# Kernel tuning notes

Measured on AMD Instinct MI355X. Metric: run time of the kernel, lower is better.

Reference implementation:

```python
import jax, jax.numpy as jnp
import numpy as np

B, F, O = 32, 26, 20
IN, G = 2048, 512
REL = 53
EPS = 1e-5  # BatchNorm1d default eps


def setup_inputs() -> dict:
    key = jax.random.key(0)
    ks = jax.random.split(key, 10)
    inp = {
        "region_feats": jax.random.normal(ks[0], (B, F, O, IN), jnp.float32),
        "region_masks": jnp.ones((B, F, O), jnp.float32),
        "rel_feats": jax.random.randint(ks[1], (B, F, O, O), 0, REL, jnp.int64),
        "tem_feats": jax.random.uniform(ks[2], (B, F * O, F * O), jnp.float32),
        # learned params (eval mode: dropout off, BN uses running stats)
        "rel_W": jax.random.normal(ks[3], (G, IN), jnp.float32) * (1.0 / np.sqrt(IN)),
        "rel_b": jnp.zeros((G,), jnp.float32),
        "rel_emb": jax.random.normal(ks[4], (REL, G), jnp.float32) * 0.02,
        "tem_W": jax.random.normal(ks[5], (G, IN), jnp.float32) * (1.0 / np.sqrt(IN)),
        "tem_b": jnp.zeros((G,), jnp.float32),
        "bn_w": jnp.ones((F * O,), jnp.float32),
        "bn_b": jnp.zeros((F * O,), jnp.float32),
        "bn_rm": jnp.zeros((F * O,), jnp.float32),
        "bn_rv": jnp.ones((F * O,), jnp.float32),
    }
    return inp


def reference(region_feats, region_masks, rel_feats, tem_feats,
              rel_W, rel_b, rel_emb, tem_W, tem_b,
              bn_w, bn_b, bn_rm, bn_rv):
    b, f, o, _ = region_feats.shape
    # ---- RELATIONAL FEATURE GRAPH ----
    # [B,F,O,G]
    rel_region = jnp.einsum("bfoi,gi->bfog", region_feats, rel_W) + rel_b
    # embedding lookup: [B,F,O,O,G]
    emb = rel_emb[rel_feats]
    mask = (rel_feats > 0).astype(region_feats.dtype)  # [B,F,O,O]
    msum = jnp.sum(mask, axis=3)                        # [B,F,O]
    # sum_j mask_ij * emb_ij  (masked reduction over neighbor dim)
    emb_sum = jnp.einsum("bfijg,bfij->bfig", emb, mask)
    # sum_j mask_ij * r_i == r_i * msum_i, so (emb_sum + r*msum)/msum
    rel_out = (emb_sum + rel_region * msum[..., None]) / msum[..., None]
    rel_out = rel_out.reshape(b, f * o, -1)
    # ---- TEMPORAL FEATURE GRAPH ----
    tem_region = jnp.einsum("bfoi,gi->bfog", region_feats, tem_W) + tem_b
    tem_region = tem_region.reshape(b, f * o, -1)
    tem_sum = jnp.sum(tem_feats, axis=2)                # [B, F*O]
    tem_out = jnp.matmul(tem_feats, tem_region) / tem_sum[..., None]
    # ---- OUTPUT ----
    out = jnp.concatenate([rel_out, tem_out], axis=-1)  # [B, F*O, 2G]
    out = jnp.tanh(out)
    # BatchNorm1d over channel dim 1 (eval mode, running stats)
    inv = bn_w / jnp.sqrt(bn_rv + EPS)                  # [F*O]
    out = (out - bn_rm[None, :, None]) * inv[None, :, None] + bn_b[None, :, None]
    return out
```

## Files before the change

### kernel.cpp

```cpp
#include <hip/hip_runtime.h>
#include <stdint.h>

#define BB 32
#define FO 520
#define M1 16640
#define KIN 2048
#define KA 2112
#define N1 1024
#define GG 512
#define K2P 576
#define M2 640

typedef unsigned short u16;
typedef short v8s __attribute__((ext_vector_type(8)));
typedef float v4f __attribute__((ext_vector_type(4)));

__device__ __forceinline__ u16 f2bf(float f) {
  union { float f; unsigned u; } v; v.f = f;
  unsigned r = v.u + 0x7fffu + ((v.u >> 16) & 1u);
  return (u16)(r >> 16);
}

__device__ __forceinline__ float fast_tanh(float x) {
  float cx = fminf(fmaxf(x, -15.f), 15.f);
  float e = __expf(2.f * cx);
  return (e - 1.f) / (e + 1.f);
}

__device__ __forceinline__ void glds(const u16* g, u16* l) {
  __builtin_amdgcn_global_load_lds((const __attribute__((address_space(1))) void*)g,
                                   (__attribute__((address_space(3))) void*)l, 16, 0, 0);
}

#define PREP_ROWS 8832
__global__ __launch_bounds__(512) void prep_all_kernel(
    const float* __restrict__ rf, const int* __restrict__ rel,
    const float* __restrict__ relW, const float* __restrict__ temW,
    const float* __restrict__ emb, const float* __restrict__ tem,
    u16* __restrict__ A1, u16* __restrict__ Wc,
    u16* __restrict__ A2, float* __restrict__ tsum) {
  const int blk = blockIdx.x;
  const int t = threadIdx.x;
  if (blk < PREP_ROWS) {
    const int row = blk * 2 + (t >> 8);
    const int tt = t & 255;
    const float* src;
    u16* orow;
    if (row < M1) { src = rf + (size_t)row * KIN; orow = A1 + (size_t)row * KA; }
    else {
      const int n = row - M1;
      src = (n < GG) ? (relW + (size_t)n * KIN) : (temW + (size_t)(n - GG) * KIN);
      orow = Wc + (size_t)n * KA;
    }
    const v4f* p = (const v4f*)src;
    v4f a = __builtin_nontemporal_load(p + 2 * tt);
    v4f b = __builtin_nontemporal_load(p + 2 * tt + 1);
    v8s v;
    v[0] = (short)f2bf(a[0]); v[1] = (short)f2bf(a[1]);
    v[2] = (short)f2bf(a[2]); v[3] = (short)f2bf(a[3]);
    v[4] = (short)f2bf(b[0]); v[5] = (short)f2bf(b[1]);
    v[6] = (short)f2bf(b[2]); v[7] = (short)f2bf(b[3]);
    *(v8s*)(orow + tt * 8) = v;
    if (tt < 64) {
      float sval = 0.f;
      if (row < M1) {
        const int* rp = rel + (size_t)row * 20;
        int cnt = 0, ms = 0;
#pragma unroll
        for (int j = 0; j < 20; ++j) { int ix = rp[j]; cnt += (ix == tt + 1); ms += (ix > 0); }
        if (tt < 52 && ms > 0) sval = (float)cnt / (float)ms;
      } else {
        const int n = row - M1;
        if (n < GG && tt < 52) sval = emb[(size_t)(tt + 1) * GG + n];
      }
      orow[KIN + tt] = f2bf(sval);
    }
    return;
  }
  const int w = t >> 6, l = t & 63;
  const int row = (blk - PREP_ROWS) * 8 + w;
  const int b = row / M2, i = row % M2;
  u16* orow = A2 + (size_t)row * K2P;
  v8s z = {0, 0, 0, 0, 0, 0, 0, 0};
  if (i >= FO) {
    *(v8s*)(orow + l * 8) = z;
    if (l < 8) *(v8s*)(orow + (64 + l) * 8) = z;
    return;
  }
  const float* srow = tem + ((size_t)b * FO + i) * FO;
  float s = 0.f;
  {
    v4f a = __builtin_nontemporal_load((const v4f*)(srow + 8 * l));
    v4f bb = __builtin_nontemporal_load((const v4f*)(srow + 8 * l + 4));
    s += a[0] + a[1] + a[2] + a[3] + bb[0] + bb[1] + bb[2] + bb[3];
    v8s v;
    v[0] = (short)f2bf(a[0]); v[1] = (short)f2bf(a[1]);
    v[2] = (short)f2bf(a[2]); v[3] = (short)f2bf(a[3]);
    v[4] = (short)f2bf(bb[0]); v[5] = (short)f2bf(bb[1]);
    v[6] = (short)f2bf(bb[2]); v[7] = (short)f2bf(bb[3]);
    *(v8s*)(orow + l * 8) = v;
  }
  if (l < 8) {
    if (l == 0) {
      v4f a = __builtin_nontemporal_load((const v4f*)(srow + 512));
      v4f bb = __builtin_nontemporal_load((const v4f*)(srow + 516));
      s += a[0] + a[1] + a[2] + a[3] + bb[0] + bb[1] + bb[2] + bb[3];
      v8s v;
      v[0] = (short)f2bf(a[0]); v[1] = (short)f2bf(a[1]);
      v[2] = (short)f2bf(a[2]); v[3] = (short)f2bf(a[3]);
      v[4] = (short)f2bf(bb[0]); v[5] = (short)f2bf(bb[1]);
      v[6] = (short)f2bf(bb[2]); v[7] = (short)f2bf(bb[3]);
      *(v8s*)(orow + 512) = v;
    } else {
      *(v8s*)(orow + (64 + l) * 8) = z;
    }
  }
#pragma unroll
  for (int off = 32; off > 0; off >>= 1) s += __shfl_down(s, off);
  if (l == 0) tsum[(size_t)b * FO + i] = s;
}

#define G1_STAGE(DST)                                                                            \
  do {                                                                                           \
    u16* dst_ = smem + (DST) + tid * 8;                                                          \
    glds(ga0, dst_);         glds(ga1, dst_ + 2048);                                             \
    glds(ga2, dst_ + 4096);  glds(ga3, dst_ + 6144);                                             \
    glds(gb0, dst_ + 8192);  glds(gb1, dst_ + 10240);                                            \
    ga0 += 32; ga1 += 32; ga2 += 32; ga3 += 32; gb0 += 32; gb1 += 32;                            \
  } while (0)

#define G1_COMPUTE(CB)                                                                           \
  do {                                                                                           \
    const u16* As_ = smem + (CB) * 12288;                                                        \
    const u16* Bs_ = As_ + 8192;                                                                 \
    v8s af[8], bf[4];                                                                            \
    _Pragma("unroll") for (int i = 0; i < 8; ++i) {                                              \
      const int ra = wm * 128 + i * 16 + r16;                                                    \
      af[i] = *(const v8s*)&As_[ra * 32 + ((quad ^ ((ra >> 1) & 3)) * 8)];                       \
    }                                                                                            \
    _Pragma("unroll") for (int j = 0; j < 4; ++j) {                                              \
      const int rb = wn * 64 + j * 16 + r16;                                                     \
      bf[j] = *(const v8s*)&Bs_[rb * 32 + ((quad ^ ((rb >> 1) & 3)) * 8)];                       \
    }                                                                                            \
    _Pragma("unroll") for (int i = 0; i < 8; ++i)                                                \
      _Pragma("unroll") for (int j = 0; j < 4; ++j)                                              \
        acc[i][j] =                                                                              \
            __builtin_amdgcn_mfma_f32_16x16x32_bf16(af[i], bf[j], acc[i][j], 0, 0, 0);           \
  } while (0)

__global__ __launch_bounds__(256, 2) void gemm1_kernel(
    const u16* __restrict__ A, const u16* __restrict__ Wc,
    const float* __restrict__ rel_b, const float* __restrict__ tem_b,
    const float* __restrict__ bn_w, const float* __restrict__ bn_b,
    const float* __restrict__ bn_rm, const float* __restrict__ bn_rv,
    float* __restrict__ out, u16* __restrict__ BT) {
  __shared__ u16 smem[36864];
  const int tid = threadIdx.x;
  const int lane = tid & 63;
  const int wv = tid >> 6, wm = wv >> 1, wn = wv & 1;
  const int id = blockIdx.x;
  const int wgid = (id & 7) * 65 + (id >> 3);
  const int mt = wgid >> 3, nt = wgid & 7;
  const int m0 = mt * 256, n0 = nt * 128;
  const int quad = lane >> 4, r16 = lane & 15;

  const u16 *ga0, *ga1, *ga2, *ga3, *gb0, *gb1;
  {
    const int r0 = tid >> 2, sl0 = tid & 3;
    const int c0 = (sl0 ^ ((r0 >> 1) & 3)) * 8;
    ga0 = A + (size_t)(m0 + r0) * KA + c0;
    ga1 = A + (size_t)(m0 + 64 + r0) * KA + c0;
    ga2 = A + (size_t)(m0 + 128 + r0) * KA + c0;
    ga3 = A + (size_t)(m0 + 192 + r0) * KA + c0;
    gb0 = Wc + (size_t)(n0 + r0) * KA + c0;
    gb1 = Wc + (size_t)(n0 + 64 + r0) * KA + c0;
  }

  v4f acc[8][4];
#pragma unroll
  for (int i = 0; i < 8; ++i)
#pragma unroll
    for (int j = 0; j < 4; ++j) { v4f z = {0.f, 0.f, 0.f, 0.f}; acc[i][j] = z; }

  G1_STAGE(0);
  G1_STAGE(12288);

  int cb = 0, nb = 2;
  for (int t = 0; t < 64; ++t) {
    G1_STAGE(nb * 12288);
    asm volatile("s_waitcnt vmcnt(12)" ::: "memory");
    __builtin_amdgcn_s_barrier();
    G1_COMPUTE(cb);
    asm volatile("s_waitcnt lgkmcnt(0)" ::: "memory");
    __builtin_amdgcn_s_barrier();
    cb = (cb == 2) ? 0 : cb + 1;
    nb = (nb == 2) ? 0 : nb + 1;
  }
  {
    const int cb1 = (cb == 2) ? 0 : cb + 1;
    asm volatile("s_waitcnt vmcnt(6)" ::: "memory");
    __builtin_amdgcn_s_barrier();
    G1_COMPUTE(cb);
    asm volatile("s_waitcnt vmcnt(0) lgkmcnt(0)" ::: "memory");
    __builtin_amdgcn_s_barrier();
    G1_COMPUTE(cb1);
  }

  if (n0 < GG) {
#pragma unroll
    for (int mtt = 0; mtt < 8; ++mtt) {
      const int mb = m0 + wm * 128 + mtt * 16 + quad * 4;
      const int bb = mb / FO;
      const int fo0 = mb - bb * FO;
      float inv[4], rm[4], bofs[4];
#pragma unroll
      for (int r = 0; r < 4; ++r) {
        const int fo = fo0 + r;
        inv[r] = bn_w[fo] * rsqrtf(bn_rv[fo] + 1e-5f);
        rm[r] = bn_rm[fo]; bofs[r] = bn_b[fo];
      }
#pragma unroll
      for (int ntt = 0; ntt < 4; ++ntt) {
        const int n = n0 + wn * 64 + ntt * 16 + r16;
        const float rbn = rel_b[n];
#pragma unroll
        for (int r = 0; r < 4; ++r) {
          float val = (fast_tanh(acc[mtt][ntt][r] + rbn) - rm[r]) * inv[r] + bofs[r];
          __builtin_nontemporal_store(val, out + (size_t)(mb + r) * N1 + n);
        }
      }
    }
  } else {
    __syncthreads();
#pragma unroll
    for (int p = 0; p < 2; ++p) {
      if (p) __syncthreads();
      if (wn == p) {
#pragma unroll
        for (int mtt = 0; mtt < 8; ++mtt) {
          const int il = wm * 128 + mtt * 16 + quad * 4;
#pragma unroll
          for (int ntt = 0; ntt < 4; ++ntt) {
            const int gl = ntt * 16 + r16;
            const float tb = tem_b[(n0 - GG) + p * 64 + gl];
            ushort4 w;
            w.x = f2bf(acc[mtt][ntt][0] + tb);
            w.y = f2bf(acc[mtt][ntt][1] + tb);
            w.z = f2bf(acc[mtt][ntt][2] + tb);
            w.w = f2bf(acc[mtt][ntt][3] + tb);
            *(ushort4*)&smem[gl * 264 + il] = w;
          }
        }
      }
      __syncthreads();
#pragma unroll
      for (int pass = 0; pass < 8; ++pass) {
        const int gl = pass * 8 + (tid >> 5);
        const int ch = tid & 31;
        const int m = m0 + ch * 8;
        const int b1 = m / FO;
        const int i1 = m - b1 * FO;
        v8s val = *(const v8s*)&smem[gl * 264 + ch * 8];
        const int g = (n0 - GG) + p * 64 + gl;
        *(v8s*)(BT + ((size_t)(b1 * GG + g)) * K2P + i1) = val;
      }
    }
  }
}

#define G2_STAGE(DST)                                                                            \
  do {                                                                                           \
    u16* dst_ = smem + (DST);                                                                    \
    glds(ga0, dst_ + lofA0); glds(gb0, dst_ + lofB0); glds(gb1, dst_ + lofB1);                   \
    ga0 += 32; gb0 += 32; gb1 += 32;                                                             \
  } while (0)

#define G2_COMPUTE(CB)                                                                           \
  do {                                                                                           \
    const u16* As_ = smem + (CB) * 12288;                                                        \
    const u16* Bs_ = As_ + 4096;                                                                 \
    v8s af[4], bf[4];                                                                            \
    _Pragma("unroll") for (int t4 = 0; t4 < 4; ++t4) {                                           \
      const int ra = wm * 64 + t4 * 16 + r16;                                                    \
      const int rb = wn * 64 + t4 * 16 + r16;                                                    \
      af[t4] = *(const v8s*)&As_[ra * 32 + ((quad ^ ((ra >> 1) & 3)) * 8)];                      \
      bf[t4] = *(const v8s*)&Bs_[rb * 32 + ((quad ^ ((rb >> 1) & 3)) * 8)];                      \
    }                                                                                            \
    _Pragma("unroll") for (int mtt = 0; mtt < 4; ++mtt)                                          \
      _Pragma("unroll") for (int ntt = 0; ntt < 4; ++ntt)                                        \
        acc[mtt][ntt] =                                                                          \
            __builtin_amdgcn_mfma_f32_16x16x32_bf16(af[mtt], bf[ntt], acc[mtt][ntt], 0, 0, 0);   \
  } while (0)

__global__ __launch_bounds__(512, 4) void gemm2_kernel(
    const u16* __restrict__ A2, const u16* __restrict__ BT,
    const float* __restrict__ tsum,
    const float* __restrict__ bn_w, const float* __restrict__ bn_b,
    const float* __restrict__ bn_rm, const float* __restrict__ bn_rv,
    float* __restrict__ out) {
  __shared__ u16 smem[36864];
  const int tid = threadIdx.x;
  const int lane = tid & 63;
  const int wv = tid >> 6, wm = wv >> 2, wn = wv & 3;
  const int m0 = blockIdx.x * 128;
  const int n0 = blockIdx.y * 256;
  const int b = blockIdx.z;
  const u16* Ab = A2 + (size_t)b * M2 * K2P;
  const u16* Bb = BT + (size_t)b * GG * K2P;
  const int quad = lane >> 4, r16 = lane & 15;

  const u16 *ga0, *gb0, *gb1;
  {
    const int r0 = tid >> 2, sl0 = tid & 3;
    const int c0 = (sl0 ^ ((r0 >> 1) & 3)) * 8;
    ga0 = Ab + (size_t)(m0 + r0) * K2P + c0;
    gb0 = Bb + (size_t)(n0 + r0) * K2P + c0;
    gb1 = Bb + (size_t)(n0 + 128 + r0) * K2P + c0;
  }
  const int lofA0 = wv * 512;
  const int lofB0 = 4096 + wv * 512;
  const int lofB1 = 8192 + wv * 512;

  v4f acc[4][4];
#pragma unroll
  for (int i = 0; i < 4; ++i)
#pragma unroll
    for (int j = 0; j < 4; ++j) { v4f z = {0.f, 0.f, 0.f, 0.f}; acc[i][j] = z; }

  G2_STAGE(0);
  G2_STAGE(12288);

  int cb = 0, nb = 2;
  for (int t = 0; t < 16; ++t) {
    G2_STAGE(nb * 12288);
    asm volatile("s_waitcnt vmcnt(6)" ::: "memory");
    __builtin_amdgcn_s_barrier();
    G2_COMPUTE(cb);
    asm volatile("s_waitcnt lgkmcnt(0)" ::: "memory");
    __builtin_amdgcn_s_barrier();
    cb = (cb == 2) ? 0 : cb + 1;
    nb = (nb == 2) ? 0 : nb + 1;
  }
  {
    const int cb1 = (cb == 2) ? 0 : cb + 1;
    asm volatile("s_waitcnt vmcnt(3)" ::: "memory");
    __builtin_amdgcn_s_barrier();
    G2_COMPUTE(cb);
    asm volatile("s_waitcnt vmcnt(0) lgkmcnt(0)" ::: "memory");
    __builtin_amdgcn_s_barrier();
    G2_COMPUTE(cb1);
  }

#pragma unroll
  for (int mtt = 0; mtt < 4; ++mtt) {
    const int ibase = m0 + wm * 64 + mtt * 16 + quad * 4;
    if (ibase >= FO) continue;
    float ts[4], inv[4], rm[4], bofs[4];
#pragma unroll
    for (int r = 0; r < 4; ++r) {
      const int i = ibase + r;
      ts[r] = 1.f / tsum[(size_t)b * FO + i];
      inv[r] = bn_w[i] * rsqrtf(bn_rv[i] + 1e-5f);
      rm[r] = bn_rm[i]; bofs[r] = bn_b[i];
    }
#pragma unroll
    for (int ntt = 0; ntt < 4; ++ntt) {
      const int g = n0 + wn * 64 + ntt * 16 + r16;
#pragma unroll
      for (int r = 0; r < 4; ++r) {
        float val = (fast_tanh(acc[mtt][ntt][r] * ts[r]) - rm[r]) * inv[r] + bofs[r];
        __builtin_nontemporal_store(val, out + ((size_t)(b * FO + (ibase + r))) * N1 + GG + g);
      }
    }
  }
}

extern "C" void kernel_launch(void* const* d_in, const int* in_sizes, int n_in,
                              void* d_out, int out_size, void* d_ws, size_t ws_size,
                              hipStream_t stream) {
  const float* region_feats = (const float*)d_in[0];
  const int* rel_feats = (const int*)d_in[2];
  const float* tem_feats = (const float*)d_in[3];
  const float* rel_W = (const float*)d_in[4];
  const float* rel_b = (const float*)d_in[5];
  const float* rel_emb = (const float*)d_in[6];
  const float* tem_W = (const float*)d_in[7];
  const float* tem_b = (const float*)d_in[8];
  const float* bn_w = (const float*)d_in[9];
  const float* bn_b = (const float*)d_in[10];
  const float* bn_rm = (const float*)d_in[11];
  const float* bn_rv = (const float*)d_in[12];
  float* out = (float*)d_out;

  char* base = (char*)d_ws;
  u16* A1 = (u16*)base;
  u16* Wc = (u16*)(base + 70287360);
  u16* A2 = (u16*)(base + 74612736);
  u16* BT = (u16*)(base + 98205696);
  float* tsum = (float*)(base + 117080064);

  prep_all_kernel<<<PREP_ROWS + 2560, 512, 0, stream>>>(
      region_feats, rel_feats, rel_W, tem_W, rel_emb, tem_feats, A1, Wc, A2, tsum);
  gemm1_kernel<<<520, 256, 0, stream>>>(A1, Wc, rel_b, tem_b,
                                        bn_w, bn_b, bn_rm, bn_rv, out, BT);
  gemm2_kernel<<<dim3(5, 2, 32), 512, 0, stream>>>(A2, BT, tsum,
                                                   bn_w, bn_b, bn_rm, bn_rv, out);
}
```

Before: 398.3 us.

## Retile gemm1 to 512-thread blocks with half-height tail tiles

```diff
diff --git a/kernel.cpp b/kernel.cpp
--- a/kernel.cpp
+++ b/kernel.cpp
@@ -120,77 +120,77 @@
   if (l == 0) tsum[(size_t)b * FO + i] = s;
 }
 
-#define G1_STAGE(DST)                                                                            \
-  do {                                                                                           \
-    u16* dst_ = smem + (DST) + tid * 8;                                                          \
-    glds(ga0, dst_);         glds(ga1, dst_ + 2048);                                             \
-    glds(ga2, dst_ + 4096);  glds(ga3, dst_ + 6144);                                             \
-    glds(gb0, dst_ + 8192);  glds(gb1, dst_ + 10240);                                            \
-    ga0 += 32; ga1 += 32; ga2 += 32; ga3 += 32; gb0 += 32; gb1 += 32;                            \
-  } while (0)
-
-#define G1_COMPUTE(CB)                                                                           \
-  do {                                                                                           \
-    const u16* As_ = smem + (CB) * 12288;                                                        \
-    const u16* Bs_ = As_ + 8192;                                                                 \
-    v8s af[8], bf[4];                                                                            \
-    _Pragma("unroll") for (int i = 0; i < 8; ++i) {                                              \
-      const int ra = wm * 128 + i * 16 + r16;                                                    \
-      af[i] = *(const v8s*)&As_[ra * 32 + ((quad ^ ((ra >> 1) & 3)) * 8)];                       \
-    }                                                                                            \
-    _Pragma("unroll") for (int j = 0; j < 4; ++j) {                                              \
-      const int rb = wn * 64 + j * 16 + r16;                                                     \
-      bf[j] = *(const v8s*)&Bs_[rb * 32 + ((quad ^ ((rb >> 1) & 3)) * 8)];                       \
-    }                                                                                            \
-    _Pragma("unroll") for (int i = 0; i < 8; ++i)                                                \
-      _Pragma("unroll") for (int j = 0; j < 4; ++j)                                              \
-        acc[i][j] =                                                                              \
-            __builtin_amdgcn_mfma_f32_16x16x32_bf16(af[i], bf[j], acc[i][j], 0, 0, 0);           \
-  } while (0)
-
-__global__ __launch_bounds__(256, 2) void gemm1_kernel(
+template <int G>
+__device__ __forceinline__ void gemm1_body(
     const u16* __restrict__ A, const u16* __restrict__ Wc,
     const float* __restrict__ rel_b, const float* __restrict__ tem_b,
     const float* __restrict__ bn_w, const float* __restrict__ bn_b,
     const float* __restrict__ bn_rm, const float* __restrict__ bn_rv,
-    float* __restrict__ out, u16* __restrict__ BT) {
-  __shared__ u16 smem[36864];
+    float* __restrict__ out, u16* __restrict__ BT, u16* smem,
+    const int m0, const int n0) {
+  constexpr int SB = (G + 1) * 4096;
   const int tid = threadIdx.x;
   const int lane = tid & 63;
   const int wv = tid >> 6, wm = wv >> 1, wn = wv & 1;
-  const int id = blockIdx.x;
-  const int wgid = (id & 7) * 65 + (id >> 3);
-  const int mt = wgid >> 3, nt = wgid & 7;
-  const int m0 = mt * 256, n0 = nt * 128;
   const int quad = lane >> 4, r16 = lane & 15;
 
-  const u16 *ga0, *ga1, *ga2, *ga3, *gb0, *gb1;
+  const u16 *ga0, *ga1 = nullptr, *gb0;
   {
     const int r0 = tid >> 2, sl0 = tid & 3;
     const int c0 = (sl0 ^ ((r0 >> 1) & 3)) * 8;
     ga0 = A + (size_t)(m0 + r0) * KA + c0;
-    ga1 = A + (size_t)(m0 + 64 + r0) * KA + c0;
-    ga2 = A + (size_t)(m0 + 128 + r0) * KA + c0;
-    ga3 = A + (size_t)(m0 + 192 + r0) * KA + c0;
+    if constexpr (G == 2) ga1 = A + (size_t)(m0 + 128 + r0) * KA + c0;
     gb0 = Wc + (size_t)(n0 + r0) * KA + c0;
-    gb1 = Wc + (size_t)(n0 + 64 + r0) * KA + c0;
-  }
-
-  v4f acc[8][4];
-#pragma unroll
-  for (int i = 0; i < 8; ++i)
+  }
+  const int lofA0 = wv * 512;
+  const int lofA1 = 4096 + wv * 512;
+  const int lofB0 = G * 4096 + wv * 512;
+
+  auto STAGE = [&](int dstoff) {
+    u16* dst_ = smem + dstoff;
+    glds(ga0, dst_ + lofA0);
+    if constexpr (G == 2) { glds(ga1, dst_ + lofA1); ga1 += 32; }
+    glds(gb0, dst_ + lofB0);
+    ga0 += 32; gb0 += 32;
+  };
+
+  v4f acc[2 * G][4];
+#pragma unroll
+  for (int i = 0; i < 2 * G; ++i)
 #pragma unroll
     for (int j = 0; j < 4; ++j) { v4f z = {0.f, 0.f, 0.f, 0.f}; acc[i][j] = z; }
 
-  G1_STAGE(0);
-  G1_STAGE(12288);
+  auto COMPUTE = [&](int cbuf) {
+    const u16* As_ = smem + cbuf * SB;
+    const u16* Bs_ = As_ + G * 4096;
+    v8s af[2 * G], bf[4];
+#pragma unroll
+    for (int i = 0; i < 2 * G; ++i) {
+      const int ra = wm * (G * 32) + i * 16 + r16;
+      af[i] = *(const v8s*)&As_[ra * 32 + ((quad ^ ((ra >> 1) & 3)) * 8)];
+    }
+#pragma unroll
+    for (int j = 0; j < 4; ++j) {
+      const int rb = wn * 64 + j * 16 + r16;
+      bf[j] = *(const v8s*)&Bs_[rb * 32 + ((quad ^ ((rb >> 1) & 3)) * 8)];
+    }
+#pragma unroll
+    for (int i = 0; i < 2 * G; ++i)
+#pragma unroll
+      for (int j = 0; j < 4; ++j)
+        acc[i][j] = __builtin_amdgcn_mfma_f32_16x16x32_bf16(af[i], bf[j], acc[i][j], 0, 0, 0);
+  };
+
+  STAGE(0);
+  STAGE(SB);
 
   int cb = 0, nb = 2;
   for (int t = 0; t < 64; ++t) {
-    G1_STAGE(nb * 12288);
-    asm volatile("s_waitcnt vmcnt(12)" ::: "memory");
-    __builtin_amdgcn_s_barrier();
-    G1_COMPUTE(cb);
+    STAGE(nb * SB);
+    if constexpr (G == 2) asm volatile("s_waitcnt vmcnt(6)" ::: "memory");
+    else                  asm volatile("s_waitcnt vmcnt(4)" ::: "memory");
+    __builtin_amdgcn_s_barrier();
+    COMPUTE(cb);
     asm volatile("s_waitcnt lgkmcnt(0)" ::: "memory");
     __builtin_amdgcn_s_barrier();
     cb = (cb == 2) ? 0 : cb + 1;
@@ -198,18 +198,19 @@
   }
   {
     const int cb1 = (cb == 2) ? 0 : cb + 1;
-    asm volatile("s_waitcnt vmcnt(6)" ::: "memory");
-    __builtin_amdgcn_s_barrier();
-    G1_COMPUTE(cb);
+    if constexpr (G == 2) asm volatile("s_waitcnt vmcnt(3)" ::: "memory");
+    else                  asm volatile("s_waitcnt vmcnt(2)" ::: "memory");
+    __builtin_amdgcn_s_barrier();
+    COMPUTE(cb);
     asm volatile("s_waitcnt vmcnt(0) lgkmcnt(0)" ::: "memory");
     __builtin_amdgcn_s_barrier();
-    G1_COMPUTE(cb1);
+    COMPUTE(cb1);
   }
 
   if (n0 < GG) {
 #pragma unroll
-    for (int mtt = 0; mtt < 8; ++mtt) {
-      const int mb = m0 + wm * 128 + mtt * 16 + quad * 4;
+    for (int mtt = 0; mtt < 2 * G; ++mtt) {
+      const int mb = m0 + wm * (G * 32) + mtt * 16 + quad * 4;
       const int bb = mb / FO;
       const int fo0 = mb - bb * FO;
       float inv[4], rm[4], bofs[4];
@@ -231,14 +232,15 @@
       }
     }
   } else {
+    constexpr int SP = G * 128 + 8;
     __syncthreads();
 #pragma unroll
     for (int p = 0; p < 2; ++p) {
       if (p) __syncthreads();
       if (wn == p) {
 #pragma unroll
-        for (int mtt = 0; mtt < 8; ++mtt) {
-          const int il = wm * 128 + mtt * 16 + quad * 4;
+        for (int mtt = 0; mtt < 2 * G; ++mtt) {
+          const int il = wm * (G * 32) + mtt * 16 + quad * 4;
 #pragma unroll
           for (int ntt = 0; ntt < 4; ++ntt) {
             const int gl = ntt * 16 + r16;
@@ -248,23 +250,56 @@
             w.y = f2bf(acc[mtt][ntt][1] + tb);
             w.z = f2bf(acc[mtt][ntt][2] + tb);
             w.w = f2bf(acc[mtt][ntt][3] + tb);
-            *(ushort4*)&smem[gl * 264 + il] = w;
+            *(ushort4*)&smem[gl * SP + il] = w;
           }
         }
       }
       __syncthreads();
-#pragma unroll
-      for (int pass = 0; pass < 8; ++pass) {
-        const int gl = pass * 8 + (tid >> 5);
-        const int ch = tid & 31;
-        const int m = m0 + ch * 8;
-        const int b1 = m / FO;
-        const int i1 = m - b1 * FO;
-        v8s val = *(const v8s*)&smem[gl * 264 + ch * 8];
-        const int g = (n0 - GG) + p * 64 + gl;
-        *(v8s*)(BT + ((size_t)(b1 * GG + g)) * K2P + i1) = val;
-      }
-    }
+      if constexpr (G == 2) {
+#pragma unroll
+        for (int pass = 0; pass < 4; ++pass) {
+          const int gl = pass * 16 + (tid >> 5);
+          const int ch = tid & 31;
+          const int m = m0 + ch * 8;
+          const int b1 = m / FO;
+          const int i1 = m - b1 * FO;
+          v8s val = *(const v8s*)&smem[gl * SP + ch * 8];
+          const int g = (n0 - GG) + p * 64 + gl;
+          *(v8s*)(BT + ((size_t)(b1 * GG + g)) * K2P + i1) = val;
+        }
+      } else {
+#pragma unroll
+        for (int pass = 0; pass < 2; ++pass) {
+          const int gl = pass * 32 + (tid >> 4);
+          const int ch = tid & 15;
+          const int m = m0 + ch * 8;
+          const int b1 = m / FO;
+          const int i1 = m - b1 * FO;
+          v8s val = *(const v8s*)&smem[gl * SP + ch * 8];
+          const int g = (n0 - GG) + p * 64 + gl;
+          *(v8s*)(BT + ((size_t)(b1 * GG + g)) * K2P + i1) = val;
+        }
+      }
+    }
+  }
+}
+
+__global__ __launch_bounds__(512, 4) void gemm1_kernel(
+    const u16* __restrict__ A, const u16* __restrict__ Wc,
+    const float* __restrict__ rel_b, const float* __restrict__ tem_b,
+    const float* __restrict__ bn_w, const float* __restrict__ bn_b,
+    const float* __restrict__ bn_rm, const float* __restrict__ bn_rv,
+    float* __restrict__ out, u16* __restrict__ BT) {
+  __shared__ u16 smem[36864];
+  const int id = blockIdx.x;
+  if (id < 512) {
+    const int wgid = (id & 7) * 64 + (id >> 3);
+    gemm1_body<2>(A, Wc, rel_b, tem_b, bn_w, bn_b, bn_rm, bn_rv, out, BT, smem,
+                  (wgid >> 3) * 256, (wgid & 7) * 128);
+  } else {
+    const int sid = id - 512;
+    gemm1_body<1>(A, Wc, rel_b, tem_b, bn_w, bn_b, bn_rm, bn_rv, out, BT, smem,
+                  16384 + (sid >> 3) * 128, (sid & 7) * 128);
   }
 }
 
@@ -401,7 +436,7 @@
 
   prep_all_kernel<<<PREP_ROWS + 2560, 512, 0, stream>>>(
       region_feats, rel_feats, rel_W, tem_W, rel_emb, tem_feats, A1, Wc, A2, tsum);
-  gemm1_kernel<<<520, 256, 0, stream>>>(A1, Wc, rel_b, tem_b,
+  gemm1_kernel<<<528, 512, 0, stream>>>(A1, Wc, rel_b, tem_b,
                                         bn_w, bn_b, bn_rm, bn_rv, out, BT);
   gemm2_kernel<<<dim3(5, 2, 32), 512, 0, stream>>>(A2, BT, tsum,
                                                    bn_w, bn_b, bn_rm, bn_rv, out);
```

After: 375.5 us. 1.06x faster.
